# Kernel tuning notes

Hardware: AMD Instinct MI355X
Metric: run time of the kernel (lower is better)

Reference implementation:

```python
import jax, jax.numpy as jnp
import numpy as np

B, S, D = 4, 4096, 1024
H = 16
DH = D // H  # 64, required by the fused kernel


def setup_inputs() -> dict:
    key = jax.random.key(0)
    ks = jax.random.split(key, 5)
    scale = 1.0 / np.sqrt(D)  # xavier-ish init scale for square matrices
    return {
        "x": jax.random.normal(ks[0], (B, S, D), dtype=jnp.float32),
        "Wq": jax.random.normal(ks[1], (D, D), dtype=jnp.float32) * scale,
        "Wk": jax.random.normal(ks[2], (D, D), dtype=jnp.float32) * scale,
        "Wv": jax.random.normal(ks[3], (D, D), dtype=jnp.float32) * scale,
        "Wo": jax.random.normal(ks[4], (D, D), dtype=jnp.float32) * scale,
    }


def reference(x, Wq, Wk, Wv, Wo):
    # Fused QKV projection + linear (non-softmax) attention.
    # Q = x Wq, K = x Wk, V = x Wv, split into H heads of size DH.
    b, s, d = x.shape
    h, dh = H, d // H

    def to_heads(t):
        return t.reshape(b, s, h, dh).transpose(0, 2, 1, 3)  # [B,H,S,dh]

    q = to_heads(jnp.einsum("bsd,de->bse", x, Wq))
    k = to_heads(jnp.einsum("bsd,de->bse", x, Wk))
    v = to_heads(jnp.einsum("bsd,de->bse", x, Wv))

    # Linear attention: O(S * dh^2) per head, never materializes [S,S].
    # out = (1/sqrt(dh)) * Q @ (K^T V)
    scale = 1.0 / jnp.sqrt(jnp.asarray(dh, dtype=x.dtype))
    kv = jnp.einsum("bhsd,bhse->bhde", k, v)          # [B,H,dh,dh]
    out = jnp.einsum("bhsd,bhde->bhse", q, kv) * scale  # [B,H,S,dh]

    # kernel output [B,H,S,dh] -> transpose(1,2) -> view [B,S,D]
    out = out.transpose(0, 2, 1, 3).reshape(b, s, d)
    # out_proj: nn.Linear(D, D, bias=False) -> x @ W.T
    return jnp.einsum("bsd,ed->bse", out, Wo)
```

## Files before the change

### kernel.cpp

```cpp
#include <hip/hip_runtime.h>

typedef unsigned short u16;
typedef unsigned int u32;
typedef u16 u16x8 __attribute__((ext_vector_type(8)));
typedef u16 u16x4 __attribute__((ext_vector_type(4)));
typedef __bf16 bf16x8 __attribute__((ext_vector_type(8)));
typedef float f32x4 __attribute__((ext_vector_type(4)));

__device__ __forceinline__ u16 f2bf(float f) {
    u32 u = __builtin_bit_cast(u32, f);
    u32 r = (u + 0x7fffu + ((u >> 16) & 1u)) >> 16;
    return (u16)r;
}
__device__ __forceinline__ void async16(const u16* g, u16* lds_base) {
    __builtin_amdgcn_global_load_lds(
        (const __attribute__((address_space(1))) void*)g,
        (__attribute__((address_space(3))) void*)lds_base, 16, 0, 0);
}
template <bool SW>
__device__ __forceinline__ f32x4 mf(bf16x8 a, bf16x8 b, f32x4 c) {
    if constexpr (SW) return __builtin_amdgcn_mfma_f32_16x16x32_bf16(b, a, c, 0, 0, 0);
    else              return __builtin_amdgcn_mfma_f32_16x16x32_bf16(a, b, c, 0, 0, 0);
}

#define BAR __builtin_amdgcn_s_barrier()
#define WAITLGK do { asm volatile("s_waitcnt lgkmcnt(0)" ::: "memory"); \
                     __builtin_amdgcn_sched_barrier(0); } while (0)
#define PRIO1 __builtin_amdgcn_s_setprio(1)
#define PRIO0 __builtin_amdgcn_s_setprio(0)
#define VM(n) asm volatile("s_waitcnt vmcnt(" #n ")" ::: "memory")

__global__ __launch_bounds__(256) void prep(
    const float* __restrict__ x, u16* __restrict__ xb, u16* __restrict__ xbT,
    const float* __restrict__ wq, u16* __restrict__ wqb,
    const float* __restrict__ wo, u16* __restrict__ wob,
    const float* __restrict__ wk, const float* __restrict__ wv,
    u16* __restrict__ WkvT) {
    const int bid = blockIdx.x;
    const int t = threadIdx.x;
    if (bid < 16384) {
        __shared__ u16 tile[32][33];
        const int s0 = (bid >> 5) * 32, n0 = (bid & 31) * 32;
        const int tx = t & 31, ty = t >> 5;
#pragma unroll
        for (int r = 0; r < 4; ++r) {
            const int s = s0 + ty + 8 * r;
            const u16 bv = f2bf(x[(size_t)s * 1024 + n0 + tx]);
            xb[(size_t)s * 1024 + n0 + tx] = bv;
            tile[ty + 8 * r][tx] = bv;
        }
        __syncthreads();
        const int b = s0 >> 12;
        const int sl = s0 & 4095;
#pragma unroll
        for (int r = 0; r < 4; ++r) {
            const int n = n0 + ty + 8 * r;
            xbT[((size_t)b * 1024 + n) * 4096 + sl + tx] = tile[tx][ty + 8 * r];
        }
    } else if (bid < 17408) {
        const int b2 = bid - 16384;
        const float* src = b2 < 512 ? wq : wo;
        u16* dst = b2 < 512 ? wqb : wob;
        const long base = b2 < 512 ? b2 : b2 - 512;
        const long idx = (base * 256 + t) * 8;
        float4 a = *(const float4*)(src + idx);
        float4 b = *(const float4*)(src + idx + 4);
        u16x8 o;
        o[0] = f2bf(a.x); o[1] = f2bf(a.y); o[2] = f2bf(a.z); o[3] = f2bf(a.w);
        o[4] = f2bf(b.x); o[5] = f2bf(b.y); o[6] = f2bf(b.z); o[7] = f2bf(b.w);
        *(u16x8*)(dst + idx) = o;
    } else {
        __shared__ float tf[32][33];
        const int b3 = bid - 17408;
        const float* W = (b3 >> 10) == 0 ? wk : wv;
        const int n0 = (b3 & 31) * 32, k0 = ((b3 >> 5) & 31) * 32;
        const int tx = t & 31, ty = t >> 5;
#pragma unroll
        for (int r = 0; r < 4; ++r)
            tf[ty + 8 * r][tx] = W[(size_t)(k0 + ty + 8 * r) * 1024 + n0 + tx];
        __syncthreads();
#pragma unroll
        for (int r = 0; r < 4; ++r) {
            const int n = n0 + ty + 8 * r;
            WkvT[((size_t)(b3 >> 10) * 1024 + n) * 1024 + k0 + tx] =
                f2bf(tf[tx][ty + 8 * r]);
        }
    }
}

__global__ __launch_bounds__(512, 1) void gemmS(
    const u16* __restrict__ A, int lda,
    const u16* __restrict__ Bt, int ldb,
    u16* __restrict__ C, int ldc, int K, int nTN,
    size_t aMask, size_t btStrideB) {
    __shared__ u16 SM[4][2][128 * 64];
    const int tid = threadIdx.x, wid = tid >> 6, lane = tid & 63;
    const int wm = wid >> 2, wn = wid & 3;

    const int nwg = gridDim.x;
    const int orig = blockIdx.x;
    const int id = (orig & 7) * (nwg >> 3) + (orig >> 3);
    const size_t mBase = (size_t)(id / nTN) * 128;
    const size_t nBase = (size_t)(id % nTN) * 128;
    const size_t mA = mBase & aMask;
    Bt += (mBase >> 10) * btStrideB;

    const int srow = lane >> 3;
    const int scol = ((lane & 7) ^ (srow & 7)) * 8;

    auto stageS = [&](int buf, int kt) {
#pragma unroll
        for (int c = 0; c < 2; ++c) {
            const u16* g = c ? Bt : A;
            const int ld = c ? ldb : lda;
            const size_t rb = c ? nBase : mA;
            u16* lds = SM[buf][c];
#pragma unroll
            for (int j = 0; j < 2; ++j) {
                const int rowL = wid * 16 + j * 8;
                async16(g + (rb + rowL + srow) * (size_t)ld + (size_t)kt * 64 + scol,
                        lds + rowL * 64);
            }
        }
    };

    const int frow = lane & 15;
    const int xs0 = ((lane >> 4) ^ (frow & 7)) * 8;
    const int xs1 = ((4 + (lane >> 4)) ^ (frow & 7)) * 8;
    f32x4 acc[4][2] = {};

    const int nk = K >> 6;
    stageS(0, 0); stageS(1, 1); stageS(2, 2);
    VM(8);
    BAR;

    for (int kt = 0; kt < nk; ++kt) {
        const int cur = kt & 3;
        if (kt + 3 < nk) stageS((kt + 3) & 3, kt + 3);
        bf16x8 aF[4][2], bF[2][2];
#pragma unroll
        for (int mi = 0; mi < 4; ++mi) {
            const int rA = (wm * 64 + mi * 16 + frow) * 64;
            aF[mi][0] = *(const bf16x8*)&SM[cur][0][rA + xs0];
            aF[mi][1] = *(const bf16x8*)&SM[cur][0][rA + xs1];
        }
#pragma unroll
        for (int ni = 0; ni < 2; ++ni) {
            const int rB = (wn * 32 + ni * 16 + frow) * 64;
            bF[ni][0] = *(const bf16x8*)&SM[cur][1][rB + xs0];
            bF[ni][1] = *(const bf16x8*)&SM[cur][1][rB + xs1];
        }
        WAITLGK;
        PRIO1;
#pragma unroll
        for (int mi = 0; mi < 4; ++mi)
#pragma unroll
            for (int ni = 0; ni < 2; ++ni)
#pragma unroll
                for (int s = 0; s < 2; ++s)
                    acc[mi][ni] = mf<true>(aF[mi][s], bF[ni][s], acc[mi][ni]);
        PRIO0;
        if (kt + 3 < nk)      { VM(8); }
        else if (kt + 2 < nk) { VM(4); }
        else if (kt + 1 < nk) { VM(0); }
        BAR;
    }

    const int rb4 = (lane >> 4) * 4, cx = lane & 15;
#pragma unroll
    for (int mi = 0; mi < 4; ++mi) {
        const size_t row = mBase + wm * 64 + mi * 16 + cx;
#pragma unroll
        for (int ni = 0; ni < 2; ++ni) {
            const size_t col = nBase + wn * 32 + ni * 16 + rb4;
            u16x4 v;
            v[0] = f2bf(acc[mi][ni][0]); v[1] = f2bf(acc[mi][ni][1]);
            v[2] = f2bf(acc[mi][ni][2]); v[3] = f2bf(acc[mi][ni][3]);
            *(u16x4*)&C[row * (size_t)ldc + col] = v;
        }
    }
}

#define As SM[0]
#define Bs SM[1]

#define LDA(buf, mh) do { _Pragma("unroll") for (int mi = 0; mi < 4; ++mi) { \
    const int rA = (wm * 128 + (mh) * 64 + mi * 16 + frow) * 64; \
    aF[mi][0] = *(const bf16x8*)&As[buf][rA + xs0]; \
    aF[mi][1] = *(const bf16x8*)&As[buf][rA + xs1]; } } while (0)

#define LDB(buf, nh) do { _Pragma("unroll") for (int ni = 0; ni < 2; ++ni) { \
    const int rB = (wn * 64 + (nh) * 32 + ni * 16 + frow) * 64; \
    bF[(nh) * 2 + ni][0] = *(const bf16x8*)&Bs[buf][rB + xs0]; \
    bF[(nh) * 2 + ni][1] = *(const bf16x8*)&Bs[buf][rB + xs1]; } } while (0)

#define MFQ(mh, nh) do { _Pragma("unroll") for (int mi = 0; mi < 4; ++mi) \
  _Pragma("unroll") for (int ni = 0; ni < 2; ++ni) \
  _Pragma("unroll") for (int s = 0; s < 2; ++s) \
    acc[(mh) * 4 + mi][(nh) * 2 + ni] = mf<true>( \
        aF[mi][s], bF[(nh) * 2 + ni][s], acc[(mh) * 4 + mi][(nh) * 2 + ni]); } while (0)

#define TILE4(buf, S2, S3, S4, W1, W2, WV) \
  LDA(buf, 0); LDB(buf, 0); BAR; WAITLGK; PRIO1; MFQ(0, 0); PRIO0; W1; BAR; \
  LDB(buf, 1); S2; BAR; WAITLGK; PRIO1; MFQ(0, 1); PRIO0; W2; BAR; \
  LDA(buf, 1); S3; BAR; WAITLGK; PRIO1; MFQ(1, 1); PRIO0; BAR; \
  S4; BAR; WAITLGK; PRIO1; MFQ(1, 0); PRIO0; WV; BAR;

__global__ __launch_bounds__(512, 2) void gemm8p(
    const u16* __restrict__ A, int lda,
    const u16* __restrict__ Bt, int ldb,
    float* __restrict__ Cq, int ldc, int K, int nTN,
    size_t btStrideB) {
    __shared__ u16 SM[2][2][256 * 64];
    const int tid = threadIdx.x;
    const int wid = tid >> 6, lane = tid & 63;
    const int wm = wid >> 2, wn = wid & 3;

    const int nwg = gridDim.x;
    const int orig = blockIdx.x;
    const int id = (orig & 7) * (nwg >> 3) + (orig >> 3);
    const size_t mBase = (size_t)(id / nTN) * 256;
    const size_t nBase = (size_t)(id % nTN) * 256;

    Bt += (mBase >> 12) * btStrideB;

    const int srow = lane >> 3;
    const int scol = (((lane & 7) ^ (srow & 7)) * 8);

    auto stageH = [&](int buf, int isB, int h, int kt) {
        const u16* g = isB ? Bt : A;
        const int ld = isB ? ldb : lda;
        const size_t rb = isB ? nBase : mBase;
        u16* lds = isB ? Bs[buf] : As[buf];
#pragma unroll
        for (int j = 0; j < 2; ++j) {
            const int rowL = isB ? ((wid >> 1) * 64 + h * 32 + (wid & 1) * 16 + j * 8)
                                 : ((wid >> 2) * 128 + h * 64 + (wid & 3) * 16 + j * 8);
            async16(g + (rb + rowL + srow) * (size_t)ld + (size_t)kt * 64 + scol,
                    lds + rowL * 64);
        }
    };

    const int frow = lane & 15;
    const int xs0 = (((lane >> 4)) ^ (frow & 7)) * 8;
    const int xs1 = ((4 + (lane >> 4)) ^ (frow & 7)) * 8;

    f32x4 acc[8][4] = {};
    bf16x8 aF[4][2], bF[4][2];

#pragma unroll
    for (int h = 0; h < 2; ++h) { stageH(0, 0, h, 0); stageH(0, 1, h, 0); }
#pragma unroll
    for (int h = 0; h < 2; ++h) { stageH(1, 0, h, 1); stageH(1, 1, h, 1); }
    VM(8);
    BAR;

    const int np = K >> 7;
    for (int p = 0; p < np - 1; ++p) {
        const int k2 = 2 * p + 2, k3 = 2 * p + 3;
        TILE4(0,
              { stageH(0, 0, 0, k2); stageH(0, 1, 0, k2); },
              stageH(0, 1, 1, k2),
              stageH(0, 0, 1, k2),
              VM(10), VM(12), VM(12));
        TILE4(1,
              { stageH(1, 0, 0, k3); stageH(1, 1, 0, k3); },
              stageH(1, 1, 1, k3),
              stageH(1, 0, 1, k3),
              VM(10), VM(12), VM(12));
    }
    TILE4(0, , , , , , VM(0));
    TILE4(1, , , , , , );

    const int rb4 = (lane >> 4) * 4;
    const int cx = lane & 15;
#pragma unroll
    for (int m = 0; m < 8; ++m) {
        const size_t row = mBase + wm * 128 + m * 16 + cx;
#pragma unroll
        for (int n = 0; n < 4; ++n) {
            const size_t col = nBase + wn * 64 + n * 16 + rb4;
            *(float4*)&Cq[row * (size_t)ldc + col] = *(float4*)&acc[m][n];
        }
    }
}

__global__ __launch_bounds__(256, 2) void kvw2(
    const u16* __restrict__ M1v, const u16* __restrict__ WvT,
    const u16* __restrict__ Wob, u16* __restrict__ W2t) {
    __shared__ u16 Ks[64 * 64];
    __shared__ u16 Vs[64 * 64];
    __shared__ u16 kvs[64 * 64];
    __shared__ u16 Aw[256 * 64];
    const int h = blockIdx.x, b = blockIdx.y;
    const int tid = threadIdx.x, w = tid >> 6, lane = tid & 63;
    const int srow = lane >> 3;
    const int scol = ((lane & 7) ^ srow) * 8;
    const int frow = lane & 15;
    const int xs0 = ((lane >> 4) ^ (frow & 7)) * 8;
    const int xs1 = ((4 + (lane >> 4)) ^ (frow & 7)) * 8;
    const u16* Ap = M1v + (size_t)b * 1048576 + (size_t)h * 64 * 1024;
    const u16* Bp = WvT + (size_t)h * 64 * 1024;
    f32x4 acc[4] = {};
    for (int kk = 0; kk < 16; ++kk) {
        __syncthreads();
#pragma unroll
        for (int j = 0; j < 2; ++j) {
            const int row = w * 16 + j * 8;
            async16(Ap + (size_t)(row + srow) * 1024 + kk * 64 + scol, &Ks[row * 64]);
            async16(Bp + (size_t)(row + srow) * 1024 + kk * 64 + scol, &Vs[row * 64]);
        }
        VM(0);
        __syncthreads();
        bf16x8 a0 = *(const bf16x8*)&Ks[(w * 16 + frow) * 64 + xs0];
        bf16x8 a1 = *(const bf16x8*)&Ks[(w * 16 + frow) * 64 + xs1];
#pragma unroll
        for (int n = 0; n < 4; ++n) {
            bf16x8 b0 = *(const bf16x8*)&Vs[(n * 16 + frow) * 64 + xs0];
            bf16x8 b1 = *(const bf16x8*)&Vs[(n * 16 + frow) * 64 + xs1];
            acc[n] = mf<false>(a0, b0, acc[n]);
            acc[n] = mf<false>(a1, b1, acc[n]);
        }
    }
    {
        const int rb4 = (lane >> 4) * 4, cx = lane & 15;
#pragma unroll
        for (int n = 0; n < 4; ++n) {
            const int col = n * 16 + cx;
            const int unit = col >> 3;
#pragma unroll
            for (int r = 0; r < 4; ++r) {
                const int row = w * 16 + rb4 + r;
                const int byteoff = row * 128 + (((unit ^ (row & 7)) << 4) | ((col & 7) << 1));
                *(u16*)((char*)kvs + byteoff) = f2bf(acc[n][r] * 0.125f);
            }
        }
    }
    __syncthreads();
    u16* outB = W2t + (size_t)b * 1048576;
    for (int eT = 0; eT < 4; ++eT) {
#pragma unroll
        for (int j = 0; j < 8; ++j) {
            const int row = w * 64 + j * 8;
            async16(Wob + (size_t)(eT * 256 + row + srow) * 1024 + h * 64 + scol,
                    &Aw[row * 64]);
        }
        VM(0);
        __syncthreads();
        f32x4 a2[4][4] = {};
#pragma unroll
        for (int m = 0; m < 4; ++m) {
            bf16x8 a0 = *(const bf16x8*)&Aw[(w * 64 + m * 16 + frow) * 64 + xs0];
            bf16x8 a1 = *(const bf16x8*)&Aw[(w * 64 + m * 16 + frow) * 64 + xs1];
#pragma unroll
            for (int n = 0; n < 4; ++n) {
                bf16x8 b0 = *(const bf16x8*)&kvs[(n * 16 + frow) * 64 + xs0];
                bf16x8 b1 = *(const bf16x8*)&kvs[(n * 16 + frow) * 64 + xs1];
                a2[m][n] = mf<false>(a0, b0, a2[m][n]);
                a2[m][n] = mf<false>(a1, b1, a2[m][n]);
            }
        }
        const int rb4 = (lane >> 4) * 4, cx = lane & 15;
#pragma unroll
        for (int m = 0; m < 4; ++m)
#pragma unroll
            for (int n = 0; n < 4; ++n)
#pragma unroll
                for (int r = 0; r < 4; ++r)
                    outB[(size_t)(eT * 256 + w * 64 + m * 16 + rb4 + r) * 1024 +
                         h * 64 + n * 16 + cx] = f2bf(a2[m][n][r]);
        __syncthreads();
    }
}

extern "C" void kernel_launch(void* const* d_in, const int* in_sizes, int n_in,
                              void* d_out, int out_size, void* d_ws, size_t ws_size,
                              hipStream_t stream) {
    const float* x  = (const float*)d_in[0];
    const float* Wq = (const float*)d_in[1];
    const float* Wk = (const float*)d_in[2];
    const float* Wv = (const float*)d_in[3];
    const float* Wo = (const float*)d_in[4];
    float* out = (float*)d_out;
    char* ws = (char*)d_ws;

    u16* xb   = (u16*)(ws);
    u16* xbT  = (u16*)(ws + 33554432);
    u16* G    = (u16*)(ws + 67108864);
    u16* M1v  = (u16*)(ws + 75497472);
    u16* WkvT = (u16*)(ws + 83886080);
    u16* Wqb  = (u16*)(ws + 88080384);
    u16* Wob  = (u16*)(ws + 90177536);
    u16* W2t  = (u16*)(ws + 92798976);
    u16* W3T  = (u16*)(ws + 101187584);
    u16* WkT  = WkvT;
    u16* WvT  = WkvT + 1048576;

    prep<<<19456, 256, 0, stream>>>(x, xb, xbT, Wq, Wqb, Wo, Wob, Wk, Wv, WkvT);

    gemmS<<<256, 512, 0, stream>>>(xbT, 4096, xbT, 4096, G, 1024, 4096, 8,
                                   ~0ULL, 4194304ULL);
    gemmS<<<256, 512, 0, stream>>>(WkT, 1024, G, 1024, M1v, 1024, 1024, 8,
                                   1023ULL, 1048576ULL);
    kvw2<<<dim3(16, 4), 256, 0, stream>>>(M1v, WvT, Wob, W2t);
    gemmS<<<256, 512, 0, stream>>>(W2t, 1024, Wqb, 1024, W3T, 1024, 1024, 8,
                                   ~0ULL, 0ULL);
    gemm8p<<<256, 512, 0, stream>>>(xb, 1024, W3T, 1024, out, 1024, 1024, 4, 1048576ULL);
}
```

Baseline: 157.7 us.

## Replace pipelined 256x256 final GEMM with simple 128x128 single-buffered kernel

The final output GEMM drops the double-buffered, swizzled 256x256 tile kernel with priority hints and hand-scheduled waits. In its place is a plain 128x128 tile kernel with 32-wide K steps, a barrier before and after every load, no LDS swizzle, and scalar fp32 stores. This simplifies the code but gives up load/compute overlap, bank-conflict avoidance and vectorized stores. The lower per-tile data reuse is also likely to make this final GEMM slower.

Result: slower. 172.3 us (+9.3%).

```diff
diff --git a/kernel.cpp b/kernel.cpp
--- a/kernel.cpp
+++ b/kernel.cpp
@@ -181,106 +181,59 @@
     }
 }
 
-#define As SM[0]
-#define Bs SM[1]
-
-#define LDA(buf, mh) do { _Pragma("unroll") for (int mi = 0; mi < 4; ++mi) { \
-    const int rA = (wm * 128 + (mh) * 64 + mi * 16 + frow) * 64; \
-    aF[mi][0] = *(const bf16x8*)&As[buf][rA + xs0]; \
-    aF[mi][1] = *(const bf16x8*)&As[buf][rA + xs1]; } } while (0)
-
-#define LDB(buf, nh) do { _Pragma("unroll") for (int ni = 0; ni < 2; ++ni) { \
-    const int rB = (wn * 64 + (nh) * 32 + ni * 16 + frow) * 64; \
-    bF[(nh) * 2 + ni][0] = *(const bf16x8*)&Bs[buf][rB + xs0]; \
-    bF[(nh) * 2 + ni][1] = *(const bf16x8*)&Bs[buf][rB + xs1]; } } while (0)
-
-#define MFQ(mh, nh) do { _Pragma("unroll") for (int mi = 0; mi < 4; ++mi) \
-  _Pragma("unroll") for (int ni = 0; ni < 2; ++ni) \
-  _Pragma("unroll") for (int s = 0; s < 2; ++s) \
-    acc[(mh) * 4 + mi][(nh) * 2 + ni] = mf<true>( \
-        aF[mi][s], bF[(nh) * 2 + ni][s], acc[(mh) * 4 + mi][(nh) * 2 + ni]); } while (0)
-
-#define TILE4(buf, S2, S3, S4, W1, W2, WV) \
-  LDA(buf, 0); LDB(buf, 0); BAR; WAITLGK; PRIO1; MFQ(0, 0); PRIO0; W1; BAR; \
-  LDB(buf, 1); S2; BAR; WAITLGK; PRIO1; MFQ(0, 1); PRIO0; W2; BAR; \
-  LDA(buf, 1); S3; BAR; WAITLGK; PRIO1; MFQ(1, 1); PRIO0; BAR; \
-  S4; BAR; WAITLGK; PRIO1; MFQ(1, 0); PRIO0; WV; BAR;
-
-__global__ __launch_bounds__(512, 2) void gemm8p(
+__global__ __launch_bounds__(256, 2) void gemm_bt(
     const u16* __restrict__ A, int lda,
     const u16* __restrict__ Bt, int ldb,
-    float* __restrict__ Cq, int ldc, int K, int nTN,
-    size_t btStrideB) {
-    __shared__ u16 SM[2][2][256 * 64];
+    float* __restrict__ C, int ldc, int K, size_t btStrideB) {
+    __shared__ u16 As[128 * 32];
+    __shared__ u16 Bs[128 * 32];
     const int tid = threadIdx.x;
-    const int wid = tid >> 6, lane = tid & 63;
-    const int wm = wid >> 2, wn = wid & 3;
-
-    const int nwg = gridDim.x;
-    const int orig = blockIdx.x;
-    const int id = (orig & 7) * (nwg >> 3) + (orig >> 3);
-    const size_t mBase = (size_t)(id / nTN) * 256;
-    const size_t nBase = (size_t)(id % nTN) * 256;
-
+    const int w = tid >> 6, lane = tid & 63;
+    const int wr = w >> 1, wc = w & 1;
+    const size_t mBase = (size_t)blockIdx.y * 128;
+    const size_t nBase = (size_t)blockIdx.x * 128;
     Bt += (mBase >> 12) * btStrideB;
 
-    const int srow = lane >> 3;
-    const int scol = (((lane & 7) ^ (srow & 7)) * 8);
-
-    auto stageH = [&](int buf, int isB, int h, int kt) {
-        const u16* g = isB ? Bt : A;
-        const int ld = isB ? ldb : lda;
-        const size_t rb = isB ? nBase : mBase;
-        u16* lds = isB ? Bs[buf] : As[buf];
+    f32x4 acc[4][4] = {};
+
+    const int sr = lane >> 2;
+    const int sc = (lane & 3) * 8;
+
+    for (int k0 = 0; k0 < K; k0 += 32) {
+        __syncthreads();
 #pragma unroll
         for (int j = 0; j < 2; ++j) {
-            const int rowL = isB ? ((wid >> 1) * 64 + h * 32 + (wid & 1) * 16 + j * 8)
-                                 : ((wid >> 2) * 128 + h * 64 + (wid & 3) * 16 + j * 8);
-            async16(g + (rb + rowL + srow) * (size_t)ld + (size_t)kt * 64 + scol,
-                    lds + rowL * 64);
-        }
-    };
-
-    const int frow = lane & 15;
-    const int xs0 = (((lane >> 4)) ^ (frow & 7)) * 8;
-    const int xs1 = ((4 + (lane >> 4)) ^ (frow & 7)) * 8;
-
-    f32x4 acc[8][4] = {};
-    bf16x8 aF[4][2], bF[4][2];
-
-#pragma unroll
-    for (int h = 0; h < 2; ++h) { stageH(0, 0, h, 0); stageH(0, 1, h, 0); }
-#pragma unroll
-    for (int h = 0; h < 2; ++h) { stageH(1, 0, h, 1); stageH(1, 1, h, 1); }
-    VM(8);
-    BAR;
-
-    const int np = K >> 7;
-    for (int p = 0; p < np - 1; ++p) {
-        const int k2 = 2 * p + 2, k3 = 2 * p + 3;
-        TILE4(0,
-              { stageH(0, 0, 0, k2); stageH(0, 1, 0, k2); },
-              stageH(0, 1, 1, k2),
-              stageH(0, 0, 1, k2),
-              VM(10), VM(12), VM(12));
-        TILE4(1,
-              { stageH(1, 0, 0, k3); stageH(1, 1, 0, k3); },
-              stageH(1, 1, 1, k3),
-              stageH(1, 0, 1, k3),
-              VM(10), VM(12), VM(12));
-    }
-    TILE4(0, , , , , , VM(0));
-    TILE4(1, , , , , , );
-
-    const int rb4 = (lane >> 4) * 4;
+            int row = w * 32 + j * 16;
+            async16(A + (mBase + row + sr) * (size_t)lda + k0 + sc, &As[row * 32]);
+            async16(Bt + (nBase + row + sr) * (size_t)ldb + k0 + sc, &Bs[row * 32]);
+        }
+        __syncthreads();
+        bf16x8 a[4], b[4];
+#pragma unroll
+        for (int m = 0; m < 4; ++m)
+            a[m] = *(const bf16x8*)&As[(wr * 64 + m * 16 + (lane & 15)) * 32 + (lane >> 4) * 8];
+#pragma unroll
+        for (int n = 0; n < 4; ++n)
+            b[n] = *(const bf16x8*)&Bs[(wc * 64 + n * 16 + (lane & 15)) * 32 + (lane >> 4) * 8];
+#pragma unroll
+        for (int m = 0; m < 4; ++m)
+#pragma unroll
+            for (int n = 0; n < 4; ++n)
+                acc[m][n] = mf<false>(a[m], b[n], acc[m][n]);
+    }
+
+    const int rb = (lane >> 4) * 4;
     const int cx = lane & 15;
 #pragma unroll
-    for (int m = 0; m < 8; ++m) {
-        const size_t row = mBase + wm * 128 + m * 16 + cx;
+    for (int m = 0; m < 4; ++m) {
 #pragma unroll
         for (int n = 0; n < 4; ++n) {
-            const size_t col = nBase + wn * 64 + n * 16 + rb4;
-            *(float4*)&Cq[row * (size_t)ldc + col] = *(float4*)&acc[m][n];
+            size_t col = nBase + wc * 64 + n * 16 + cx;
+#pragma unroll
+            for (int r = 0; r < 4; ++r) {
+                size_t row = mBase + wr * 64 + m * 16 + rb + r;
+                C[row * (size_t)ldc + col] = acc[m][n][r];
+            }
         }
     }
 }
@@ -405,5 +358,6 @@
     kvw2<<<dim3(16, 4), 256, 0, stream>>>(M1v, WvT, Wob, W2t);
     gemmS<<<256, 512, 0, stream>>>(W2t, 1024, Wqb, 1024, W3T, 1024, 1024, 8,
                                    ~0ULL, 0ULL);
-    gemm8p<<<256, 512, 0, stream>>>(xb, 1024, W3T, 1024, out, 1024, 1024, 4, 1048576ULL);
-}
+    gemm_bt<<<dim3(8, 128), 256, 0, stream>>>(xb, 1024, W3T, 1024, out, 1024, 1024,
+                                              1048576ULL);
+}
```
